# Kernel optimization log

Hardware: AMD Instinct MI355X
Metric: run time of the kernel (lower is better)

## Reference

```python
import jax, jax.numpy as jnp
import numpy as np

S, B, D, H, V, TOK = 512, 32, 512, 512, 64, 30000
L = 2  # num LSTM layers


def _lstm_dir(x, Wih, Whh, bih, bhh, reverse):
    # x: [S, B, Din]; Wih: [4H, Din]; Whh: [4H, H]
    Bn = x.shape[1]
    Hn = Whh.shape[1]

    def step(carry, xt):
        h, c = carry
        g = xt @ Wih.T + h @ Whh.T + bih + bhh  # [B, 4H]
        i, f, gg, o = jnp.split(g, 4, axis=-1)  # torch gate order i,f,g,o
        c = jax.nn.sigmoid(f) * c + jax.nn.sigmoid(i) * jnp.tanh(gg)
        h = jax.nn.sigmoid(o) * jnp.tanh(c)
        return (h, c), h

    init = (jnp.zeros((Bn, Hn), x.dtype), jnp.zeros((Bn, Hn), x.dtype))
    _, hs = jax.lax.scan(step, init, x, reverse=reverse)
    return hs  # [S, B, H], time-aligned with x


def _bilstm(x, Wih0, Whh0, bih0, bhh0, Wih1, Whh1, bih1, bhh1):
    # layer 0
    hf = _lstm_dir(x, Wih0[0], Whh0[0], bih0[0], bhh0[0], reverse=False)
    hb = _lstm_dir(x, Wih0[1], Whh0[1], bih0[1], bhh0[1], reverse=True)
    x = jnp.concatenate([hf, hb], axis=-1)  # [S, B, 2H]
    # layer 1
    hf = _lstm_dir(x, Wih1[0], Whh1[0], bih1[0], bhh1[0], reverse=False)
    hb = _lstm_dir(x, Wih1[1], Whh1[1], bih1[1], bhh1[1], reverse=True)
    return jnp.concatenate([hf, hb], axis=-1)  # [S, B, 2H]


def setup_inputs() -> dict:
    key = jax.random.key(0)
    ks = jax.random.split(key, 16)
    s = 0.05
    inp = {}
    inp['source'] = jax.random.randint(ks[0], (S, B), 0, TOK)
    inp['target'] = jax.random.randint(ks[1], (S, B), 0, V)
    inp['emb'] = jax.random.normal(ks[2], (TOK, D), jnp.float32) * s
    inp['Wih0'] = jax.random.normal(ks[3], (2, 4 * H, D), jnp.float32) * s
    inp['Whh0'] = jax.random.normal(ks[4], (2, 4 * H, H), jnp.float32) * s
    inp['bih0'] = jax.random.normal(ks[5], (2, 4 * H), jnp.float32) * s
    inp['bhh0'] = jax.random.normal(ks[6], (2, 4 * H), jnp.float32) * s
    inp['Wih1'] = jax.random.normal(ks[7], (2, 4 * H, 2 * H), jnp.float32) * s
    inp['Whh1'] = jax.random.normal(ks[8], (2, 4 * H, H), jnp.float32) * s
    inp['bih1'] = jax.random.normal(ks[9], (2, 4 * H), jnp.float32) * s
    inp['bhh1'] = jax.random.normal(ks[10], (2, 4 * H), jnp.float32) * s
    inp['Wout'] = jax.random.normal(ks[11], (V, 2 * H), jnp.float32) * s
    inp['bout'] = jax.random.normal(ks[12], (V,), jnp.float32) * s
    inp['trans'] = jax.random.uniform(ks[13], (V, V), jnp.float32)  # torch.rand
    return inp


def reference(source, target, emb, Wih0, Whh0, bih0, bhh0, Wih1, Whh1, bih1, bhh1, Wout, bout, trans):
    # get_logits: frozen embedding -> BiLSTM -> linear
    x = jax.lax.stop_gradient(emb[source])  # [S, B, D] (embedding under no_grad)
    h = _bilstm(x, Wih0, Whh0, bih0, bhh0, Wih1, Whh1, bih1, bhh1)  # [S, B, 2H]
    logits = (h @ Wout.T + bout)[:, 0, :]  # [S, V] -- forward() decodes batch 0

    # Viterbi: max-plus recurrence over time
    def vstep(delta, lt):
        scores = delta[:, None] + trans + lt[None, :]  # [V_prev, V_cur]
        return jnp.max(scores, axis=0), jnp.argmax(scores, axis=0)

    delta, bps = jax.lax.scan(vstep, logits[0], logits[1:])  # bps: [S-1, V]
    last = jnp.argmax(delta)

    def back(idx, bp):
        prev = bp[idx]
        return prev, prev

    _, rev = jax.lax.scan(back, last, bps, reverse=True)  # rev[t] = tag at t, t in [0, S-2]
    path = jnp.concatenate([rev, last[None]]).astype(jnp.int32)  # [S]
    return path
```

## Files before the change

kernel.cpp:

```cpp
#include <hip/hip_runtime.h>
#include <stdint.h>

constexpr int kS = 512;
constexpr int kB = 32;
constexpr int kH = 512;
constexpr int kV = 64;


__device__ __forceinline__ float fast_sigmoid(float x) {
  return __builtin_amdgcn_rcpf(1.0f + __expf(-x));
}
__device__ __forceinline__ float fast_tanh(float x) {
  return 1.0f - 2.0f * __builtin_amdgcn_rcpf(1.0f + __expf(2.0f * x));
}
__device__ __forceinline__ float bcast(float v, int k) {
  return __uint_as_float(__builtin_amdgcn_readlane(__float_as_uint(v), k));
}
__device__ __forceinline__ unsigned ld_mall_nowait(const unsigned* p) {
  unsigned r;
  asm volatile("global_load_dword %0, %1, off sc0 sc1" : "=v"(r) : "v"(p));
  return r;
}
__device__ __forceinline__ void wait_vm0(unsigned& r) {
  asm volatile("s_waitcnt vmcnt(0)" : "+v"(r)::"memory");
}
__device__ __forceinline__ unsigned ld_mall(const unsigned* p) {
  unsigned r;
  asm volatile("global_load_dword %0, %1, off sc0 sc1\n\ts_waitcnt vmcnt(0)"
               : "=v"(r) : "v"(p) : "memory");
  return r;
}

__global__ __launch_bounds__(128) void k_embed(const int* __restrict__ src,
                                               const float* __restrict__ emb,
                                               float* __restrict__ X) {
  const int t = blockIdx.x;
  const int s = src[t * kB];
  const float4* e = (const float4*)(emb + (size_t)s * 512);
  float4* x = (float4*)(X + (size_t)t * 512);
  x[threadIdx.x] = e[threadIdx.x];
}

template <int KZ>
__global__ __launch_bounds__(512, 1) void k_rec(
    const float* __restrict__ Z0,
    const float* __restrict__ Z1,
    const float* __restrict__ Wih,
    const float* __restrict__ Whh,
    const float* __restrict__ bih,
    const float* __restrict__ bhh,
    float* __restrict__ Hout) {
  constexpr int ZPW = KZ / 8;
  __shared__ float part[64 * 9];
  const int bx = blockIdx.x;
  const int dir = bx & 1, wg = bx >> 1;
  const int tid = threadIdx.x;
  const int wv = tid >> 6, l = tid & 63;
  const float* WihB = Wih + (size_t)dir * 2048 * KZ;
  const float* WhhB = Whh + (size_t)dir * 2048 * 512;
  float* Hb = Hout + (size_t)dir * kS * kH;
  const int grow = (l >> 4) * 512 + wg * 16 + (l & 15);

  float ww[64];
  {
    const float* wp = WhhB + (size_t)grow * 512 + wv * 64;
#pragma unroll
    for (int i = 0; i < 64; i += 4) {
      const float4 v = *(const float4*)(wp + i);
      ww[i] = v.x; ww[i + 1] = v.y; ww[i + 2] = v.z; ww[i + 3] = v.w;
    }
  }
  float zw[ZPW];
  {
    const float* zp = WihB + (size_t)grow * KZ + wv * ZPW;
#pragma unroll
    for (int i = 0; i < ZPW; i += 4) {
      const float4 v = *(const float4*)(zp + i);
      zw[i] = v.x; zw[i + 1] = v.y; zw[i + 2] = v.z; zw[i + 3] = v.w;
    }
  }
  float bias = 0.0f;
  if (wv == 0) bias = bih[dir * 2048 + grow] + bhh[dir * 2048 + grow];
  float cstate = 0.0f;

  const float* zbase = (KZ == 512) ? Z0 : ((wv < 4) ? Z0 : Z1);
  const int zoff = (KZ == 512) ? tid : ((wv & 3) * 128 + l);

  const int t0 = dir ? (kS - 1) : 0;
  float zc0 = zbase[(size_t)t0 * 512 + zoff];
  float zc1 = (KZ == 1024) ? zbase[(size_t)t0 * 512 + zoff + 64] : 0.0f;

  for (int s = 0; s < kS; s++) {
    const int t = dir ? (kS - 1 - s) : s;
    int tn = dir ? (t - 1) : (t + 1);
    if (tn < 0) tn = 0;
    if (tn > kS - 1) tn = kS - 1;
    int tp = dir ? (t + 1) : (t - 1);
    if (tp < 0) tp = 0;
    if (tp > kS - 1) tp = kS - 1;
    const unsigned* hp = (const unsigned*)(Hb + (size_t)tp * kH) + tid;

    unsigned u = 0;
    if (s > 0) u = ld_mall_nowait(hp);

    const float zn0 = zbase[(size_t)tn * 512 + zoff];
    const float zn1 = (KZ == 1024) ? zbase[(size_t)tn * 512 + zoff + 64] : 0.0f;

    float a0 = 0.f, a1 = 0.f, a2 = 0.f, a3 = 0.f;
#pragma unroll
    for (int k = 0; k < 64; k += 4) {
      a0 += zw[k + 0] * bcast(zc0, k + 0);
      a1 += zw[k + 1] * bcast(zc0, k + 1);
      a2 += zw[k + 2] * bcast(zc0, k + 2);
      a3 += zw[k + 3] * bcast(zc0, k + 3);
    }
    if (KZ == 1024) {
#pragma unroll
      for (int k = 0; k < 64; k += 4) {
        a0 += zw[64 + k + 0] * bcast(zc1, k + 0);
        a1 += zw[64 + k + 1] * bcast(zc1, k + 1);
        a2 += zw[64 + k + 2] * bcast(zc1, k + 2);
        a3 += zw[64 + k + 3] * bcast(zc1, k + 3);
      }
    }

    if (s > 0) {
      wait_vm0(u);
#pragma unroll
      for (int q = 0; q < 4; q++) {
        const unsigned long long cm = 0xFFFFULL << (q * 16);
        while (__ballot(u == 0xFFFFFFFFu) & cm) {
          if (u == 0xFFFFFFFFu) u = ld_mall(hp);
        }
        const float hq = __uint_as_float(u);
#pragma unroll
        for (int k = q * 16; k < q * 16 + 16; k += 4) {
          a0 += ww[k + 0] * bcast(hq, k + 0);
          a1 += ww[k + 1] * bcast(hq, k + 1);
          a2 += ww[k + 2] * bcast(hq, k + 2);
          a3 += ww[k + 3] * bcast(hq, k + 3);
        }
      }
    }
    part[l * 9 + wv] = (a0 + a1) + (a2 + a3);
    __syncthreads();
    if (wv == 0) {
      float ssum = bias;
#pragma unroll
      for (int w = 0; w < 8; w++) ssum += part[l * 9 + w];
      const float act = (l >= 32 && l < 48) ? fast_tanh(ssum)
                                            : fast_sigmoid(ssum);
      const float fg = __shfl(act, (l + 16) & 63);
      const float gt = __shfl(act, (l + 32) & 63);
      const float og = __shfl(act, (l + 48) & 63);
      if (l < 16) {
        cstate = fg * cstate + act * gt;
        const float h = og * fast_tanh(cstate);
        __hip_atomic_store((unsigned*)(Hb + (size_t)t * kH) + wg * 16 + l,
                           __float_as_uint(h), __ATOMIC_RELAXED,
                           __HIP_MEMORY_SCOPE_AGENT);
      }
    }
    zc0 = zn0;
    zc1 = zn1;
  }
}

__global__ __launch_bounds__(256) void k_logits(const float* __restrict__ H1,
                                                const float* __restrict__ Wout,
                                                const float* __restrict__ bout,
                                                float* __restrict__ LOG) {
  __shared__ float hl[1024];
  const int t = blockIdx.x;
  const int tid = threadIdx.x;
  float4* hl4 = (float4*)hl;
  if (tid < 128)
    hl4[tid] = ((const float4*)(H1 + (size_t)t * kH))[tid];
  else
    hl4[tid] = ((const float4*)(H1 + (size_t)(kS + t) * kH))[tid - 128];
  __syncthreads();
  const int v = tid >> 2, q = tid & 3;
  const float4* w4 = (const float4*)(Wout + (size_t)v * 1024);
  float4 a = {0, 0, 0, 0};
#pragma unroll 8
  for (int j = 0; j < 64; j++) {
    const int idx = j * 4 + q;
    const float4 w = w4[idx];
    const float4 x = hl4[idx];
    a.x += w.x * x.x; a.y += w.y * x.y; a.z += w.z * x.z; a.w += w.w * x.w;
  }
  float acc = (a.x + a.y) + (a.z + a.w);
  acc += __shfl_xor(acc, 1);
  acc += __shfl_xor(acc, 2);
  if (q == 0) LOG[(size_t)t * kV + v] = acc + bout[v];
}

__global__ __launch_bounds__(256) void k_viterbi(const float* __restrict__ LOG,
                                                 const float* __restrict__ trans,
                                                 int* __restrict__ out) {
  __shared__ float delta[64];
  __shared__ float redS[4 * 64];
  __shared__ int redA[4 * 64];
  __shared__ unsigned char bp[511 * 64];
  const int tid = threadIdx.x;
  const int c = tid & 63, q = tid >> 6;
  if (tid < 64) delta[tid] = LOG[tid];
  __syncthreads();
  for (int t = 1; t < kS; t++) {
    float best = -1e30f;
    int bi = 0;
#pragma unroll 4
    for (int pp = 0; pp < 16; pp++) {
      const int p = q * 16 + pp;
      const float sc = delta[p] + trans[p * 64 + c];
      if (sc > best) { best = sc; bi = p; }
    }
    redS[q * 64 + c] = best;
    redA[q * 64 + c] = bi;
    __syncthreads();
    if (tid < 64) {
      float b = redS[c];
      int a = redA[c];
      for (int qq = 1; qq < 4; qq++) {
        const float v2 = redS[qq * 64 + c];
        if (v2 > b) { b = v2; a = redA[qq * 64 + c]; }
      }
      bp[(t - 1) * 64 + c] = (unsigned char)a;
      delta[c] = b + LOG[t * 64 + c];
    }
    __syncthreads();
  }
  if (tid == 0) {
    float b = delta[0];
    int a = 0;
    for (int i = 1; i < 64; i++)
      if (delta[i] > b) { b = delta[i]; a = i; }
    int idx = a;
    out[kS - 1] = idx;
    for (int t = kS - 2; t >= 0; t--) {
      idx = bp[t * 64 + idx];
      out[t] = idx;
    }
  }
}

extern "C" void kernel_launch(void* const* d_in, const int* in_sizes, int n_in,
                              void* d_out, int out_size, void* d_ws,
                              size_t ws_size, hipStream_t stream) {
  (void)in_sizes; (void)n_in; (void)out_size; (void)ws_size;
  const int* source  = (const int*)d_in[0];
  const float* emb   = (const float*)d_in[2];
  const float* Wih0  = (const float*)d_in[3];
  const float* Whh0  = (const float*)d_in[4];
  const float* bih0  = (const float*)d_in[5];
  const float* bhh0  = (const float*)d_in[6];
  const float* Wih1  = (const float*)d_in[7];
  const float* Whh1  = (const float*)d_in[8];
  const float* bih1  = (const float*)d_in[9];
  const float* bhh1  = (const float*)d_in[10];
  const float* Wout  = (const float*)d_in[11];
  const float* bout  = (const float*)d_in[12];
  const float* trans = (const float*)d_in[13];

  float* ws = (float*)d_ws;
  float* X   = ws;
  float* H0  = ws + 262144;
  float* H1  = ws + 786432;
  float* LOG = ws + 1310720;

  hipMemsetAsync(H0, 0xFF, (size_t)1048576 * sizeof(float), stream);

  k_embed<<<kS, 128, 0, stream>>>(source, emb, X);
  k_rec<512><<<64, 512, 0, stream>>>(X, X, Wih0, Whh0, bih0, bhh0, H0);
  k_rec<1024><<<64, 512, 0, stream>>>(H0, H0 + 262144, Wih1, Whh1, bih1, bhh1, H1);
  k_logits<<<kS, 256, 0, stream>>>(H1, Wout, bout, LOG);
  k_viterbi<<<1, 256, 0, stream>>>(LOG, trans, (int*)d_out);
}
```

Baseline: 2.127 ms.

## Pin recurrent workgroups to XCDs and synchronize via local L2 flags

The recurrent kernel now launches 256 workgroups. Each one reads its hardware XCC id and claims a slot through an atomic counter, so that each LSTM direction's 32 workgroups end up on a single XCD and the extras exit. Each hidden step is published to an L2-local buffer with per-workgroup ready flags, plus a device-scope copy. Consumers poll the local flags and read from L2 instead of doing MALL-level polling, falling back to the global path if the local path does not complete. Separately, Viterbi is rewritten as a single wavefront that keeps the transition column in registers and broadcasts delta with readlane, which drops shared-memory reductions and barriers. The risks are that XCC placement is not guaranteed and that the extra atomics and memsets add cost.

```diff
diff --git a/kernel.cpp b/kernel.cpp
--- a/kernel.cpp
+++ b/kernel.cpp
@@ -28,6 +28,21 @@
   unsigned r;
   asm volatile("global_load_dword %0, %1, off sc0 sc1\n\ts_waitcnt vmcnt(0)"
                : "=v"(r) : "v"(p) : "memory");
+  return r;
+}
+__device__ __forceinline__ unsigned ld_l2(const unsigned* p) {
+  unsigned r;
+  asm volatile("global_load_dword %0, %1, off sc0\n\ts_waitcnt vmcnt(0)"
+               : "=v"(r) : "v"(p) : "memory");
+  return r;
+}
+__device__ __forceinline__ void atomic_pub_local(unsigned* p, unsigned v) {
+  asm volatile("global_atomic_swap %0, %1, off" :: "v"(p), "v"(v) : "memory");
+}
+__device__ __forceinline__ unsigned atomic_probe_local(const unsigned* p) {
+  unsigned r, z = 0;
+  asm volatile("global_atomic_or %0, %1, %2, off sc0\n\ts_waitcnt vmcnt(0)"
+               : "=v"(r) : "v"(p), "v"(z) : "memory");
   return r;
 }
 
@@ -49,16 +64,33 @@
     const float* __restrict__ Whh,
     const float* __restrict__ bih,
     const float* __restrict__ bhh,
-    float* __restrict__ Hout) {
+    float* __restrict__ HL,
+    float* __restrict__ HG,
+    unsigned* __restrict__ FL,
+    int* __restrict__ claims) {
   constexpr int ZPW = KZ / 8;
   __shared__ float part[64 * 9];
-  const int bx = blockIdx.x;
-  const int dir = bx & 1, wg = bx >> 1;
+  __shared__ int claim_s;
   const int tid = threadIdx.x;
+
+  if (tid == 0) {
+    unsigned x;
+    asm volatile("s_getreg_b32 %0, hwreg(HW_REG_XCC_ID)" : "=s"(x));
+    x &= 7u;
+    const int r = atomicAdd(claims + x, 1);
+    claim_s = (x < 2u && r < 32) ? (int)((x << 5) | r) : -1;
+  }
+  __syncthreads();
+  const int cl = claim_s;
+  if (cl < 0) return;
+  const int dir = cl >> 5, wg = cl & 31;
+
   const int wv = tid >> 6, l = tid & 63;
   const float* WihB = Wih + (size_t)dir * 2048 * KZ;
   const float* WhhB = Whh + (size_t)dir * 2048 * 512;
-  float* Hb = Hout + (size_t)dir * kS * kH;
+  float* HbL = HL + (size_t)dir * kS * kH;
+  float* HbG = HG + (size_t)dir * kS * kH;
+  unsigned* FLb = FL + (size_t)dir * kS * 32;
   const int grow = (l >> 4) * 512 + wg * 16 + (l & 15);
 
   float ww[64];
@@ -89,6 +121,8 @@
   const int t0 = dir ? (kS - 1) : 0;
   float zc0 = zbase[(size_t)t0 * 512 + zoff];
   float zc1 = (KZ == 1024) ? zbase[(size_t)t0 * 512 + zoff + 64] : 0.0f;
+
+  int lmode = -1;
 
   for (int s = 0; s < kS; s++) {
     const int t = dir ? (kS - 1 - s) : s;
@@ -98,10 +132,12 @@
     int tp = dir ? (t + 1) : (t - 1);
     if (tp < 0) tp = 0;
     if (tp > kS - 1) tp = kS - 1;
-    const unsigned* hp = (const unsigned*)(Hb + (size_t)tp * kH) + tid;
+    const unsigned* gp = (const unsigned*)(HbG + (size_t)tp * kH) + tid;
+    const unsigned* lp = (const unsigned*)(HbL + (size_t)tp * kH) + tid;
+    const unsigned* flp = FLb + (size_t)tp * 32 + 4 * wv;
 
     unsigned u = 0;
-    if (s > 0) u = ld_mall_nowait(hp);
+    if (s > 0 && lmode != 1) u = ld_mall_nowait(gp);
 
     const float zn0 = zbase[(size_t)tn * 512 + zoff];
     const float zn1 = (KZ == 1024) ? zbase[(size_t)tn * 512 + zoff + 64] : 0.0f;
@@ -125,16 +161,71 @@
     }
 
     if (s > 0) {
-      wait_vm0(u);
-#pragma unroll
-      for (int q = 0; q < 4; q++) {
-        const unsigned long long cm = 0xFFFFULL << (q * 16);
-        while (__ballot(u == 0xFFFFFFFFu) & cm) {
-          if (u == 0xFFFFFFFFu) u = ld_mall(hp);
+      if (lmode == 1) {
+        unsigned fs = 0;
+        while (true) {
+          if (l < 4 && fs == 0) fs = atomic_probe_local(flp + l);
+          if ((__ballot(fs != 0) & 0xFull) == 0xFull) break;
+        }
+        u = ld_l2(lp);
+        int tries = 0;
+        while (__ballot(u == 0xFFFFFFFFu)) {
+          if (u == 0xFFFFFFFFu) {
+            tries++;
+            u = (tries <= 8) ? ld_l2(lp) : ld_mall(gp);
+          }
         }
         const float hq = __uint_as_float(u);
 #pragma unroll
-        for (int k = q * 16; k < q * 16 + 16; k += 4) {
+        for (int k = 0; k < 64; k += 4) {
+          a0 += ww[k + 0] * bcast(hq, k + 0);
+          a1 += ww[k + 1] * bcast(hq, k + 1);
+          a2 += ww[k + 2] * bcast(hq, k + 2);
+          a3 += ww[k + 3] * bcast(hq, k + 3);
+        }
+      } else if (lmode == 0) {
+        wait_vm0(u);
+#pragma unroll
+        for (int q = 0; q < 4; q++) {
+          const unsigned long long cm = 0xFFFFULL << (q * 16);
+          while (__ballot(u == 0xFFFFFFFFu) & cm) {
+            if (u == 0xFFFFFFFFu) u = ld_mall(gp);
+          }
+          const float hq = __uint_as_float(u);
+#pragma unroll
+          for (int k = q * 16; k < q * 16 + 16; k += 4) {
+            a0 += ww[k + 0] * bcast(hq, k + 0);
+            a1 += ww[k + 1] * bcast(hq, k + 1);
+            a2 += ww[k + 2] * bcast(hq, k + 2);
+            a3 += ww[k + 3] * bcast(hq, k + 3);
+          }
+        }
+      } else {
+        wait_vm0(u);
+        unsigned fs = 0;
+        bool local_ok = false;
+        while (true) {
+          if (l < 4 && fs == 0) fs = atomic_probe_local(flp + l);
+          if ((__ballot(fs != 0) & 0xFull) == 0xFull) { local_ok = true; break; }
+          if (__ballot(u == 0xFFFFFFFFu) == 0) break;
+          if (u == 0xFFFFFFFFu) u = ld_mall(gp);
+        }
+        if (local_ok) {
+          lmode = 1;
+          u = ld_l2(lp);
+          int tries = 0;
+          while (__ballot(u == 0xFFFFFFFFu)) {
+            if (u == 0xFFFFFFFFu) {
+              tries++;
+              u = (tries <= 8) ? ld_l2(lp) : ld_mall(gp);
+            }
+          }
+        } else {
+          lmode = 0;
+        }
+        const float hq = __uint_as_float(u);
+#pragma unroll
+        for (int k = 0; k < 64; k += 4) {
           a0 += ww[k + 0] * bcast(hq, k + 0);
           a1 += ww[k + 1] * bcast(hq, k + 1);
           a2 += ww[k + 2] * bcast(hq, k + 2);
@@ -153,12 +244,18 @@
       const float fg = __shfl(act, (l + 16) & 63);
       const float gt = __shfl(act, (l + 32) & 63);
       const float og = __shfl(act, (l + 48) & 63);
+      unsigned hv = 0;
       if (l < 16) {
         cstate = fg * cstate + act * gt;
         const float h = og * fast_tanh(cstate);
-        __hip_atomic_store((unsigned*)(Hb + (size_t)t * kH) + wg * 16 + l,
-                           __float_as_uint(h), __ATOMIC_RELAXED,
-                           __HIP_MEMORY_SCOPE_AGENT);
+        hv = __float_as_uint(h);
+        atomic_pub_local((unsigned*)(HbL + (size_t)t * kH) + wg * 16 + l, hv);
+      }
+      asm volatile("s_waitcnt vmcnt(0)" ::: "memory");
+      if (l == 0) atomic_pub_local(FLb + (size_t)t * 32 + wg, 1u);
+      if (l < 16) {
+        __hip_atomic_store((unsigned*)(HbG + (size_t)t * kH) + wg * 16 + l,
+                           hv, __ATOMIC_RELAXED, __HIP_MEMORY_SCOPE_AGENT);
       }
     }
     zc0 = zn0;
@@ -195,46 +292,49 @@
   if (q == 0) LOG[(size_t)t * kV + v] = acc + bout[v];
 }
 
-__global__ __launch_bounds__(256) void k_viterbi(const float* __restrict__ LOG,
-                                                 const float* __restrict__ trans,
-                                                 int* __restrict__ out) {
-  __shared__ float delta[64];
-  __shared__ float redS[4 * 64];
-  __shared__ int redA[4 * 64];
+__global__ __launch_bounds__(64) void k_viterbi(const float* __restrict__ LOG,
+                                                const float* __restrict__ trans,
+                                                int* __restrict__ out) {
   __shared__ unsigned char bp[511 * 64];
-  const int tid = threadIdx.x;
-  const int c = tid & 63, q = tid >> 6;
-  if (tid < 64) delta[tid] = LOG[tid];
+  const int c = threadIdx.x;
+  float tr[64];
+#pragma unroll
+  for (int p = 0; p < 64; p++) tr[p] = trans[p * 64 + c];
+  float delta = LOG[c];
+  for (int t = 1; t < kS; t++) {
+    const float lg = LOG[t * 64 + c];
+    float b0 = bcast(delta, 0) + tr[0];
+    float b1 = bcast(delta, 16) + tr[16];
+    float b2 = bcast(delta, 32) + tr[32];
+    float b3 = bcast(delta, 48) + tr[48];
+    int i0 = 0, i1 = 16, i2 = 32, i3 = 48;
+#pragma unroll
+    for (int j = 1; j < 16; j++) {
+      { const float sc = bcast(delta, j) + tr[j];
+        if (sc > b0) { b0 = sc; i0 = j; } }
+      { const float sc = bcast(delta, 16 + j) + tr[16 + j];
+        if (sc > b1) { b1 = sc; i1 = 16 + j; } }
+      { const float sc = bcast(delta, 32 + j) + tr[32 + j];
+        if (sc > b2) { b2 = sc; i2 = 32 + j; } }
+      { const float sc = bcast(delta, 48 + j) + tr[48 + j];
+        if (sc > b3) { b3 = sc; i3 = 48 + j; } }
+    }
+    float best = b0; int bi = i0;
+    if (b1 > best) { best = b1; bi = i1; }
+    if (b2 > best) { best = b2; bi = i2; }
+    if (b3 > best) { best = b3; bi = i3; }
+    bp[(t - 1) * 64 + c] = (unsigned char)bi;
+    delta = best + lg;
+  }
   __syncthreads();
-  for (int t = 1; t < kS; t++) {
-    float best = -1e30f;
-    int bi = 0;
-#pragma unroll 4
-    for (int pp = 0; pp < 16; pp++) {
-      const int p = q * 16 + pp;
-      const float sc = delta[p] + trans[p * 64 + c];
-      if (sc > best) { best = sc; bi = p; }
-    }
-    redS[q * 64 + c] = best;
-    redA[q * 64 + c] = bi;
-    __syncthreads();
-    if (tid < 64) {
-      float b = redS[c];
-      int a = redA[c];
-      for (int qq = 1; qq < 4; qq++) {
-        const float v2 = redS[qq * 64 + c];
-        if (v2 > b) { b = v2; a = redA[qq * 64 + c]; }
-      }
-      bp[(t - 1) * 64 + c] = (unsigned char)a;
-      delta[c] = b + LOG[t * 64 + c];
-    }
-    __syncthreads();
-  }
-  if (tid == 0) {
-    float b = delta[0];
-    int a = 0;
-    for (int i = 1; i < 64; i++)
-      if (delta[i] > b) { b = delta[i]; a = i; }
+  float b = bcast(delta, 0);
+  int a = 0;
+#pragma unroll
+  for (int p = 1; p < 64; p++) {
+    const float v = bcast(delta, p);
+    if (v > b) { b = v; a = p; }
+  }
+  if (c == 0) {
     int idx = a;
     out[kS - 1] = idx;
     for (int t = kS - 2; t >= 0; t--) {
@@ -264,15 +364,23 @@
 
   float* ws = (float*)d_ws;
   float* X   = ws;
-  float* H0  = ws + 262144;
-  float* H1  = ws + 786432;
-  float* LOG = ws + 1310720;
-
-  hipMemsetAsync(H0, 0xFF, (size_t)1048576 * sizeof(float), stream);
+  float* H0L = ws + 262144;
+  float* H0G = ws + 786432;
+  float* H1L = ws + 1310720;
+  float* H1G = ws + 1835008;
+  float* LOG = ws + 2359296;
+  unsigned* FL0 = (unsigned*)(ws + 2392064);
+  unsigned* FL1 = (unsigned*)(ws + 2424832);
+  int*      CLM = (int*)(ws + 2457600);
+
+  hipMemsetAsync(H0L, 0xFF, (size_t)4 * 524288 * sizeof(float), stream);
+  hipMemsetAsync(FL0, 0, (size_t)(2 * 32768 + 16) * sizeof(int), stream);
 
   k_embed<<<kS, 128, 0, stream>>>(source, emb, X);
-  k_rec<512><<<64, 512, 0, stream>>>(X, X, Wih0, Whh0, bih0, bhh0, H0);
-  k_rec<1024><<<64, 512, 0, stream>>>(H0, H0 + 262144, Wih1, Whh1, bih1, bhh1, H1);
-  k_logits<<<kS, 256, 0, stream>>>(H1, Wout, bout, LOG);
-  k_viterbi<<<1, 256, 0, stream>>>(LOG, trans, (int*)d_out);
-}
+  k_rec<512><<<256, 512, 0, stream>>>(X, X, Wih0, Whh0, bih0, bhh0,
+                                      H0L, H0G, FL0, CLM);
+  k_rec<1024><<<256, 512, 0, stream>>>(H0G, H0G + 262144, Wih1, Whh1, bih1,
+                                       bhh1, H1L, H1G, FL1, CLM + 8);
+  k_logits<<<kS, 256, 0, stream>>>(H1G, Wout, bout, LOG);
+  k_viterbi<<<1, 64, 0, stream>>>(LOG, trans, (int*)d_out);
+}
```

Result: slower. 6.193 ms (+191.2%).
